# Optimization experiments

Hardware: AMD Instinct MI355X
Metric: run time of the kernel (lower is better)

Reference implementation:

```python
import jax, jax.numpy as jnp
import numpy as np
from jax import lax

B, S, T, H, VIN, VOUT = 32, 128, 64, 512, 32000, 32000
PAD_IDX = 1


def setup_inputs() -> dict:
    key = jax.random.key(0)
    ks = jax.random.split(key, 20)
    sc = 0.05
    rn = lambda k, shp: (jax.random.normal(k, shp, jnp.float32) * sc)
    return {
        "src": jax.random.randint(ks[0], (B, S), 0, VIN),
        "src_len": jnp.full((B,), S, dtype=jnp.int32),
        "trg": jax.random.randint(ks[1], (B, T), 0, VOUT),
        "enc_emb": rn(ks[2], (VIN, H)),
        "enc_wih": rn(ks[3], (4 * H, H)),
        "enc_whh": rn(ks[4], (4 * H, H)),
        "enc_bih": rn(ks[5], (4 * H,)),
        "enc_bhh": rn(ks[6], (4 * H,)),
        "enc_fc_w": rn(ks[7], (H, H)),
        "enc_fc_b": rn(ks[8], (H,)),
        "dec_emb": rn(ks[9], (VOUT, H)),
        "attn_w": rn(ks[10], (H, 2 * H)),
        "attn_b": rn(ks[11], (H,)),
        "attn_v": rn(ks[12], (H,)),
        "dec_wih": rn(ks[13], (4 * H, 2 * H)),
        "dec_whh": rn(ks[14], (4 * H, H)),
        "dec_bih": rn(ks[15], (4 * H,)),
        "dec_bhh": rn(ks[16], (4 * H,)),
        "out_w": rn(ks[17], (VOUT, 3 * H)),
        "out_b": rn(ks[18], (VOUT,)),
    }


def _lstm_cell(x, h, c, wih, whh, bih, bhh):
    # PyTorch gate order: i, f, g, o
    g = x @ wih.T + bih + h @ whh.T + bhh
    i, f, gg, o = jnp.split(g, 4, axis=-1)
    c = jax.nn.sigmoid(f) * c + jax.nn.sigmoid(i) * jnp.tanh(gg)
    h = jax.nn.sigmoid(o) * jnp.tanh(c)
    return h, c


def reference(src, src_len, trg, enc_emb, enc_wih, enc_whh, enc_bih, enc_bhh,
              enc_fc_w, enc_fc_b, dec_emb, attn_w, attn_b, attn_v,
              dec_wih, dec_whh, dec_bih, dec_bhh, out_w, out_b):
    b = src.shape[0]
    # ---- Encoder: single-layer LSTM over time (full lengths) ----
    emb = enc_emb[src].transpose(1, 0, 2)  # [S,B,H] time-major
    h0 = jnp.zeros((b, H), emb.dtype)
    c0 = jnp.zeros((b, H), emb.dtype)

    def enc_step(carry, x_t):
        h, c = carry
        h, c = _lstm_cell(x_t, h, c, enc_wih, enc_whh, enc_bih, enc_bhh)
        return (h, c), h

    (hf, cf), enc_out = lax.scan(enc_step, (h0, c0), emb)  # enc_out [S,B,H]
    hidden = jnp.tanh(hf @ enc_fc_w.T + enc_fc_b)  # [B,H]
    enc_bt = enc_out.transpose(1, 0, 2)  # [B,S,H]
    mask = src != PAD_IDX  # [B,S]

    # ---- Decoder: teacher forcing (ratio=1.0), scan over target steps ----
    def dec_step(carry, tok):
        h, c = carry
        e = dec_emb[tok]  # [B,H]
        # Bahdanau attention
        hrep = jnp.broadcast_to(h[:, None, :], enc_bt.shape)  # [B,S,H]
        energy = jnp.tanh(jnp.concatenate([hrep, enc_bt], -1) @ attn_w.T + attn_b)
        score = energy @ attn_v  # [B,S]
        score = jnp.where(mask, score, jnp.float32(-1e10))
        a = jax.nn.softmax(score, axis=1)
        weighted = jnp.einsum('bs,bsh->bh', a, enc_bt)  # [B,H]
        x = jnp.concatenate([e, weighted], -1)  # [B,2H]
        h, c = _lstm_cell(x, h, c, dec_wih, dec_whh, dec_bih, dec_bhh)
        pred = jnp.concatenate([h, weighted, e], -1) @ out_w.T + out_b  # [B,V]
        return (h, c), pred

    tokens = trg.T  # [T,B]
    (_, _), logits = lax.scan(dec_step, (hidden, cf), tokens[:-1])  # [T-1,B,V]
    outputs = jnp.concatenate(
        [jnp.zeros((1, b, VOUT), logits.dtype), logits], axis=0)  # [T,B,V]
    return outputs
```

## Files before the change

### kernel.cpp

```cpp
#include <hip/hip_runtime.h>

typedef unsigned short u16;
typedef unsigned int u32;
typedef unsigned long long u64;
typedef __attribute__((ext_vector_type(8))) short bf16x8;
typedef __attribute__((ext_vector_type(8))) unsigned short u16x8;
typedef __attribute__((ext_vector_type(4))) unsigned short u16x4;
typedef __attribute__((ext_vector_type(4))) float f32x4;

#define DEVI static __device__ __forceinline__
#define MFMA __builtin_amdgcn_mfma_f32_16x16x32_bf16

constexpr int B = 32, S = 128, T = 64, H = 512, V = 32000;
constexpr int H4 = 4 * H;
constexpr int TD = T - 1;
constexpr int MOUT = TD * B;
constexpr int KOUT = 3 * H;
constexpr int PAD_IDX = 1;

DEVI u16 f2bf(float f) {
  union { float f; unsigned u; } v; v.f = f;
  unsigned r = (v.u + 0x7fffu + ((v.u >> 16) & 1u)) >> 16;
  return (u16)r;
}
DEVI float bf2f(u16 h) {
  union { unsigned u; float f; } v; v.u = ((unsigned)h) << 16;
  return v.f;
}
DEVI float sigm(float x) { return 1.f / (1.f + __expf(-x)); }
DEVI float tanh_(float x) {
  float ax = fabsf(x);
  float e = __expf(-2.f * ax);
  float t = (1.f - e) / (1.f + e);
  return x < 0.f ? -t : t;
}
DEVI float tanhf_(float x) {
  float e = __expf(2.f * x);
  return 1.f - 2.f * __builtin_amdgcn_rcpf(e + 1.f);
}
DEVI int swz(int row, int k8) { return row * 32 + ((k8 ^ (row & 3)) << 3); }

DEVI u64 pack4u(const u16* p) {
  return (u64)p[0] | ((u64)p[1] << 16) | ((u64)p[2] << 32) | ((u64)p[3] << 48);
}
DEVI u64 xstore(u16* p, u64 v) {
  return __hip_atomic_exchange((u64*)p, v, __ATOMIC_RELAXED,
                               __HIP_MEMORY_SCOPE_AGENT);
}
DEVI void sstore(unsigned* p, unsigned v) {
  __hip_atomic_exchange(p, v, __ATOMIC_RELAXED, __HIP_MEMORY_SCOPE_AGENT);
}
DEVI void poll_bo(unsigned* p, unsigned tgt) {
  int it = 0;
  long long t0 = (long long)__builtin_amdgcn_s_memrealtime();
  while (__hip_atomic_load(p, __ATOMIC_RELAXED, __HIP_MEMORY_SCOPE_AGENT) <
         tgt) {
    if (it < 4) {
      __builtin_amdgcn_s_sleep(1);
      it++;
    } else {
      __builtin_amdgcn_s_sleep(8);
    }
    if ((long long)__builtin_amdgcn_s_memrealtime() - t0 > 20000000ll) break;
  }
}

__global__ __launch_bounds__(256) void gemm_bt(
    const u16* __restrict__ A, int lda,
    const u16* __restrict__ Bt, int ldb,
    float* __restrict__ C, int ldc,
    const float* __restrict__ bias, int M, int K, int bf16out) {
  __shared__ u16 As[128 * 32], Bs[128 * 32];
  const int tid = threadIdx.x;
  const int m0 = blockIdx.y * 128, n0 = blockIdx.x * 128;
  const int lane = tid & 63, w = tid >> 6, wm = w >> 1, wn = w & 1;
  const int lr = lane & 15, lk = lane >> 4;
  f32x4 acc[4][4] = {};
  const int r = tid >> 1, cc = (tid & 1) * 16, k8b = (tid & 1) * 2;

  for (int k0 = 0; k0 < K; k0 += 32) {
    {
      long gr = m0 + r;
      u16x8 v0 = {}, v1 = {};
      if (gr < M) {
        const u16* s = A + gr * (long)lda + k0 + cc;
        v0 = *(const u16x8*)s;
        v1 = *(const u16x8*)(s + 8);
      }
      *(u16x8*)&As[swz(r, k8b)] = v0;
      *(u16x8*)&As[swz(r, k8b + 1)] = v1;
    }
    {
      const u16* s = Bt + (long)(n0 + r) * ldb + k0 + cc;
      u16x8 v0 = *(const u16x8*)s;
      u16x8 v1 = *(const u16x8*)(s + 8);
      *(u16x8*)&Bs[swz(r, k8b)] = v0;
      *(u16x8*)&Bs[swz(r, k8b + 1)] = v1;
    }
    __syncthreads();
    bf16x8 af[4], bfr[4];
#pragma unroll
    for (int mi = 0; mi < 4; mi++)
      af[mi] = *(const bf16x8*)&As[swz(wm * 64 + mi * 16 + lr, lk)];
#pragma unroll
    for (int ni = 0; ni < 4; ni++)
      bfr[ni] = *(const bf16x8*)&Bs[swz(wn * 64 + ni * 16 + lr, lk)];
#pragma unroll
    for (int mi = 0; mi < 4; mi++)
#pragma unroll
      for (int ni = 0; ni < 4; ni++)
        acc[mi][ni] = MFMA(af[mi], bfr[ni], acc[mi][ni], 0, 0, 0);
    __syncthreads();
  }
#pragma unroll
  for (int ni = 0; ni < 4; ni++) {
    int col = n0 + wn * 64 + ni * 16 + lr;
    float bs = bias ? bias[col] : 0.f;
#pragma unroll
    for (int mi = 0; mi < 4; mi++) {
#pragma unroll
      for (int rr = 0; rr < 4; rr++) {
        long row = m0 + wm * 64 + mi * 16 + lk * 4 + rr;
        if (row < M) {
          float v = acc[mi][ni][rr] + bs;
          if (bf16out)
            ((u16*)C)[row * (long)ldc + col] = f2bf(v);
          else
            C[row * (long)ldc + col] = v;
        }
      }
    }
  }
}

__global__ void zero_f(float* p, long n) {
  long i = (long)blockIdx.x * 256 + threadIdx.x;
  long st = (long)gridDim.x * 256;
  for (; i < n; i += st) p[i] = 0.f;
}

__global__ void zero_u(unsigned* p, int n) {
  int i = blockIdx.x * 256 + threadIdx.x;
  if (i < n) p[i] = 0u;
}

__global__ void cast_bf(const float* __restrict__ src, u16* __restrict__ dst,
                        int ld, int off, int Csz) {
  long row = blockIdx.y;
  int col = blockIdx.x * 256 + threadIdx.x;
  dst[row * Csz + col] = f2bf(src[row * ld + off + col]);
}

__global__ void cast_bf4(const float* __restrict__ src, u16* __restrict__ dst,
                         long n4) {
  long i = (long)blockIdx.x * 256 + threadIdx.x;
  if (i >= n4) return;
  float4 v = ((const float4*)src)[i];
  u16x4 o;
  o[0] = f2bf(v.x); o[1] = f2bf(v.y); o[2] = f2bf(v.z); o[3] = f2bf(v.w);
  *(u16x4*)&dst[i * 4] = o;
}

__global__ void cast_perm(const float* __restrict__ src, int ld, int off,
                          u16* __restrict__ dst) {
  int np = blockIdx.y;
  int c = blockIdx.x * 256 + threadIdx.x;
  int g = np & 3, jH = np >> 2;
  dst[(size_t)np * H + c] = f2bf(src[(size_t)(g * H + jH) * ld + off + c]);
}

__global__ void pack_wdec_p(const float* __restrict__ wih,
                            const float* __restrict__ whh,
                            u16* __restrict__ dst) {
  int r = blockIdx.y;
  int k = blockIdx.x * 256 + threadIdx.x;
  int g = r & 3, j = r >> 2;
  int srow = g * H + j;
  float v = (k < 512) ? wih[(size_t)srow * (2 * H) + 512 + k]
                      : whh[(size_t)srow * H + (k - 512)];
  dst[(size_t)r * 1024 + k] = f2bf(v);
}

__global__ void bias_perm(const float* __restrict__ a,
                          const float* __restrict__ b, float* __restrict__ o) {
  int np = blockIdx.x * 256 + threadIdx.x;
  int g = np & 3, jH = np >> 2;
  int r = g * H + jH;
  o[np] = a[r] + b[r];
}

__global__ __launch_bounds__(256) void cast_transpose_bf(
    const float* __restrict__ src, int ld, int off, u16* __restrict__ dst,
    int R) {
  __shared__ float tile[32][33];
  int r0 = blockIdx.y * 32, c0 = blockIdx.x * 32;
  int tx = threadIdx.x & 31, ty = threadIdx.x >> 5;
#pragma unroll
  for (int i = 0; i < 32; i += 8)
    tile[ty + i][tx] = src[(long)(r0 + ty + i) * ld + off + c0 + tx];
  __syncthreads();
#pragma unroll
  for (int i = 0; i < 32; i += 8)
    dst[(long)(c0 + ty + i) * R + r0 + tx] = f2bf(tile[tx][ty + i]);
}

__global__ void gather_src_emb(const int* __restrict__ src,
                               const float* __restrict__ emb,
                               u16* __restrict__ dst) {
  int row = blockIdx.y;
  int t = row >> 5, b = row & 31;
  int c = blockIdx.x * 256 + threadIdx.x;
  int tok = src[b * S + t];
  dst[(long)row * H + c] = f2bf(emb[(long)tok * H + c]);
}

__global__ void gather_trg_emb(const int* __restrict__ trg,
                               const float* __restrict__ emb,
                               u16* __restrict__ xout) {
  int row = blockIdx.y;
  int t = row >> 5, b = row & 31;
  int c = blockIdx.x * 256 + threadIdx.x;
  int tok = trg[b * T + t];
  xout[(long)row * KOUT + 2 * H + c] = f2bf(emb[(long)tok * H + c]);
}

__global__ __launch_bounds__(512) void enc_persist32(
    unsigned* fes, const u16* __restrict__ wenc_p,
    const float* __restrict__ xih_p, u16* hstep, u16* enc_bt_bf, float* cbuf) {
  __shared__ float gs[32][64];
  __shared__ float c_s[512];
  __shared__ u16 hx[512];
  const int tid = threadIdx.x, bk = blockIdx.x;
  const int wave = tid >> 6, lane = tid & 63;
  const int lr = lane & 15, lk = lane >> 4;
  const int bq = tid >> 4, jl = tid & 15;
  c_s[tid] = 0.f;
  const int mt = wave & 1, nt = wave >> 1;
  const int n = nt * 16 + lr;
  bf16x8 wf[16];
  {
    const u16* wp = wenc_p + (size_t)(bk * 64 + n) * 512 + lk * 8;
#pragma unroll
    for (int kt = 0; kt < 16; kt++) wf[kt] = *(const bf16x8*)(wp + kt * 32);
  }
  for (int t = 0; t < S; t++) {
    if (t > 0 && tid < 32) poll_bo(fes + tid * 16, (unsigned)t);
    __syncthreads();
    float4 xv = *(const float4*)(xih_p + ((size_t)t * B + bq) * H4 +
                                 (bk * 16 + jl) * 4);
    {
      const u16* ab =
          hstep + (size_t)t * B * H + (size_t)(mt * 16 + lr) * H + lk * 8;
      f32x4 acc = {};
#pragma unroll
      for (int kt = 0; kt < 16; kt++) {
        bf16x8 a = *(const bf16x8*)(ab + kt * 32);
        acc = MFMA(a, wf[kt], acc, 0, 0, 0);
      }
#pragma unroll
      for (int rr = 0; rr < 4; rr++) gs[mt * 16 + lk * 4 + rr][n] = acc[rr];
    }
    __syncthreads();
    {
      float gi = xv.x + gs[bq][jl * 4 + 0];
      float gf = xv.y + gs[bq][jl * 4 + 1];
      float gg = xv.z + gs[bq][jl * 4 + 2];
      float go = xv.w + gs[bq][jl * 4 + 3];
      float cn = sigm(gf) * c_s[tid] + sigm(gi) * tanh_(gg);
      c_s[tid] = cn;
      u16 h16 = f2bf(sigm(go) * tanh_(cn));
      hx[tid] = h16;
      enc_bt_bf[((size_t)bq * S + t) * H + bk * 16 + jl] = h16;
    }
    __syncthreads();
    u64 kp = 0;
    if (tid < 128) {
      int bb = tid >> 2, q = tid & 3;
      kp = xstore(hstep + (size_t)(t + 1) * B * H + (size_t)bb * H + bk * 16 +
                      q * 4,
                  pack4u(&hx[bb * 16 + q * 4]));
    }
    if (wave < 2) {
      asm volatile("" :: "v"(kp));
      asm volatile("s_waitcnt vmcnt(0)" ::: "memory");
    }
    __syncthreads();
    if (tid == 0) sstore(fes + bk * 16, (unsigned)(t + 1));
  }
  cbuf[bq * H + bk * 16 + jl] = c_s[tid];
}

__global__ __launch_bounds__(512) void dec_persist32(
    unsigned* fhs, unsigned* fws, const float* __restrict__ fc_w,
    const float* __restrict__ fc_b, const u16* __restrict__ wdec_p,
    const u16* __restrict__ a1T_bf, const float* __restrict__ attn_v,
    const int* __restrict__ src, const u16* __restrict__ hf_bf,
    const float* __restrict__ cbuf, const u16* __restrict__ epart_bf,
    const u16* __restrict__ enc_bt_bf, const float* __restrict__ eih_p,
    u16* hstep, u16* wstep, u16* __restrict__ xout_bf) {
  __shared__ float buf[8][512];
  __shared__ float hs[512], hps[512];
  __shared__ float gh[32][64];
  __shared__ float gw[32][64];
  __shared__ float sc[128], red[2];
  __shared__ int smask[128];
  __shared__ float c_s[512];
  __shared__ u16 hx[512];
  const int tid = threadIdx.x, bk = blockIdx.x;
  const int wave = tid >> 6, lane = tid & 63;
  const int lr = lane & 15, lk = lane >> 4;
  const int bq = tid >> 4, jl = tid & 15;
  c_s[tid] = cbuf[bq * H + bk * 16 + jl];
  if (tid < 128) smask[tid] = src[bk * S + tid];
  float av8[8];
#pragma unroll
  for (int e = 0; e < 8; e++) av8[e] = attn_v[lane * 8 + e];
  if (wave < 2) {
    const u16* ab = hf_bf + (size_t)(wave * 16 + lr) * H + lk * 8;
    const float* frow = fc_w + (size_t)(bk * 16 + lr) * H + lk * 8;
    f32x4 acc = {};
#pragma unroll
    for (int kt = 0; kt < 16; kt++) {
      bf16x8 a = *(const bf16x8*)(ab + kt * 32);
      bf16x8 w;
#pragma unroll
      for (int e = 0; e < 8; e++) w[e] = (short)f2bf(frow[kt * 32 + e]);
      acc = MFMA(a, w, acc, 0, 0, 0);
    }
    float bs = fc_b[bk * 16 + lr];
#pragma unroll
    for (int rr = 0; rr < 4; rr++)
      hx[(wave * 16 + lk * 4 + rr) * 16 + lr] = f2bf(tanh_(acc[rr] + bs));
  }
  __syncthreads();
  {
    u64 kp = 0;
    if (tid < 128) {
      int bb = tid >> 2, q = tid & 3;
      kp = xstore(hstep + (size_t)bb * H + bk * 16 + q * 4,
                  pack4u(&hx[bb * 16 + q * 4]));
    }
    if (wave < 2) {
      asm volatile("" :: "v"(kp));
      asm volatile("s_waitcnt vmcnt(0)" ::: "memory");
    }
    __syncthreads();
    if (tid == 0) sstore(fhs + bk * 16, 1u);
  }
  const int mt = wave & 1, nt = wave >> 1;
  const int n = nt * 16 + lr;
  const u16* wpw = wdec_p + (size_t)(bk * 64 + n) * 1024 + lk * 8;
  const u16* wph = wpw + 512;
  bf16x8 wwf[16];
#pragma unroll
  for (int kt = 0; kt < 16; kt++) wwf[kt] = *(const bf16x8*)(wpw + kt * 32);
  for (int t = 0; t < TD; t++) {
    if (tid < 32) poll_bo(fhs + tid * 16, (unsigned)(t + 1));
    __syncthreads();
    float4 xv = *(const float4*)(eih_p + ((size_t)t * B + bq) * H4 +
                                 (bk * 16 + jl) * 4);
    {
      const u16* ah =
          hstep + (size_t)t * B * H + (size_t)(mt * 16 + lr) * H + lk * 8;
      f32x4 acc = {};
#pragma unroll
      for (int kt = 0; kt < 16; kt++) {
        bf16x8 a = *(const bf16x8*)(ah + kt * 32);
        bf16x8 w = *(const bf16x8*)(wph + kt * 32);
        acc = MFMA(a, w, acc, 0, 0, 0);
      }
#pragma unroll
      for (int rr = 0; rr < 4; rr++) gh[mt * 16 + lk * 4 + rr][n] = acc[rr];
    }
    if (tid < 256) {
      u32 v = ((const u32*)(hstep + (size_t)t * B * H + (size_t)bk * H))[tid];
      hs[2 * tid] = bf2f((u16)(v & 0xffff));
      hs[2 * tid + 1] = bf2f((u16)(v >> 16));
    }
    __syncthreads();
    {
      float p[8] = {};
      const int j0 = lane * 8;
#pragma unroll 8
      for (int kk = 0; kk < 64; kk++) {
        int k = wave * 64 + kk;
        float hk = hs[k];
        u16x8 av = *(const u16x8*)&a1T_bf[(size_t)k * H + j0];
#pragma unroll
        for (int e = 0; e < 8; e++) p[e] += hk * bf2f(av[e]);
      }
#pragma unroll
      for (int e = 0; e < 8; e++) buf[wave][j0 + e] = p[e];
    }
    __syncthreads();
    {
      float s0 = 0.f;
#pragma unroll
      for (int w = 0; w < 8; w++) s0 += buf[w][tid];
      hps[tid] = s0;
    }
    __syncthreads();
    {
      const int j0 = lane * 8;
      float hp8[8];
#pragma unroll
      for (int e = 0; e < 8; e++) hp8[e] = hps[j0 + e];
#pragma unroll 4
      for (int i = 0; i < 16; i++) {
        int s = wave * 16 + i;
        u16x8 ep = *(const u16x8*)&epart_bf[((size_t)bk * S + s) * H + j0];
        float a = 0.f;
#pragma unroll
        for (int e = 0; e < 8; e++) a += av8[e] * tanhf_(hp8[e] + bf2f(ep[e]));
#pragma unroll
        for (int o = 32; o; o >>= 1) a += __shfl_xor(a, o);
        if (lane == 0) sc[s] = (smask[s] == PAD_IDX) ? -1e10f : a;
      }
    }
    __syncthreads();
    if (tid < 64) {
      float v = fmaxf(sc[tid], sc[tid + 64]);
#pragma unroll
      for (int o = 32; o; o >>= 1) v = fmaxf(v, __shfl_xor(v, o));
      if (tid == 0) red[0] = v;
    }
    __syncthreads();
    float mx = red[0];
    if (tid < S) sc[tid] = __expf(sc[tid] - mx);
    __syncthreads();
    if (tid < 64) {
      float v = sc[tid] + sc[tid + 64];
#pragma unroll
      for (int o = 32; o; o >>= 1) v += __shfl_xor(v, o);
      if (tid == 0) red[1] = 1.f / v;
    }
    __syncthreads();
    {
      float acc8[8] = {};
      const int j0 = lane * 8;
#pragma unroll 4
      for (int i = 0; i < 16; i++) {
        int s = wave * 16 + i;
        float ps = sc[s];
        u16x8 ev = *(const u16x8*)&enc_bt_bf[((size_t)bk * S + s) * H + j0];
#pragma unroll
        for (int e = 0; e < 8; e++) acc8[e] += ps * bf2f(ev[e]);
      }
#pragma unroll
      for (int e = 0; e < 8; e++) buf[wave][j0 + e] = acc8[e];
    }
    __syncthreads();
    {
      u64 kp = 0;
      if (tid < 128) {
        float inv = red[1];
        int j0 = tid * 4;
        u16x4 o;
#pragma unroll
        for (int i = 0; i < 4; i++) {
          float wj = (buf[0][j0 + i] + buf[1][j0 + i] + buf[2][j0 + i] +
                      buf[3][j0 + i] + buf[4][j0 + i] + buf[5][j0 + i] +
                      buf[6][j0 + i] + buf[7][j0 + i]) *
                     inv;
          o[i] = f2bf(wj);
        }
        *(u16x4*)&xout_bf[((size_t)t * B + bk) * KOUT + H + j0] = o;
        u64 val = (u64)o[0] | ((u64)o[1] << 16) | ((u64)o[2] << 32) |
                  ((u64)o[3] << 48);
        kp = xstore(wstep + ((size_t)t * B + bk) * H + j0, val);
      }
      if (wave < 2) {
        asm volatile("" :: "v"(kp));
        asm volatile("s_waitcnt vmcnt(0)" ::: "memory");
      }
      __syncthreads();
      if (tid == 0) sstore(fws + bk * 16, (unsigned)(t + 1));
    }
    if (tid < 32) poll_bo(fws + tid * 16, (unsigned)(t + 1));
    __syncthreads();
    {
      const u16* aw =
          wstep + (size_t)t * B * H + (size_t)(mt * 16 + lr) * H + lk * 8;
      f32x4 acc = {};
#pragma unroll
      for (int kt = 0; kt < 16; kt++) {
        bf16x8 a = *(const bf16x8*)(aw + kt * 32);
        acc = MFMA(a, wwf[kt], acc, 0, 0, 0);
      }
#pragma unroll
      for (int rr = 0; rr < 4; rr++) gw[mt * 16 + lk * 4 + rr][n] = acc[rr];
    }
    __syncthreads();
    {
      float gi = xv.x + gh[bq][jl * 4 + 0] + gw[bq][jl * 4 + 0];
      float gf = xv.y + gh[bq][jl * 4 + 1] + gw[bq][jl * 4 + 1];
      float gg = xv.z + gh[bq][jl * 4 + 2] + gw[bq][jl * 4 + 2];
      float go = xv.w + gh[bq][jl * 4 + 3] + gw[bq][jl * 4 + 3];
      float cn = sigm(gf) * c_s[tid] + sigm(gi) * tanh_(gg);
      c_s[tid] = cn;
      u16 h16 = f2bf(sigm(go) * tanh_(cn));
      hx[tid] = h16;
      xout_bf[((size_t)t * B + bq) * KOUT + bk * 16 + jl] = h16;
    }
    __syncthreads();
    {
      u64 kp = 0;
      if (tid < 128) {
        int bb = tid >> 2, q = tid & 3;
        kp = xstore(hstep + (size_t)(t + 1) * B * H + (size_t)bb * H +
                        bk * 16 + q * 4,
                    pack4u(&hx[bb * 16 + q * 4]));
      }
      if (wave < 2) {
        asm volatile("" :: "v"(kp));
        asm volatile("s_waitcnt vmcnt(0)" ::: "memory");
      }
      __syncthreads();
      if (tid == 0) sstore(fhs + bk * 16, (unsigned)(t + 2));
    }
  }
}

extern "C" void kernel_launch(void* const* d_in, const int* in_sizes, int n_in,
                              void* d_out, int out_size, void* d_ws,
                              size_t ws_size, hipStream_t stream) {
  const int* src = (const int*)d_in[0];
  const int* trg = (const int*)d_in[2];
  const float* enc_emb = (const float*)d_in[3];
  const float* enc_wih = (const float*)d_in[4];
  const float* enc_whh = (const float*)d_in[5];
  const float* enc_bih = (const float*)d_in[6];
  const float* enc_bhh = (const float*)d_in[7];
  const float* fc_w = (const float*)d_in[8];
  const float* fc_b = (const float*)d_in[9];
  const float* dec_emb = (const float*)d_in[10];
  const float* attn_w = (const float*)d_in[11];
  const float* attn_b = (const float*)d_in[12];
  const float* attn_v = (const float*)d_in[13];
  const float* dec_wih = (const float*)d_in[14];
  const float* dec_whh = (const float*)d_in[15];
  const float* dec_bih = (const float*)d_in[16];
  const float* dec_bhh = (const float*)d_in[17];
  const float* out_w = (const float*)d_in[18];
  const float* out_b = (const float*)d_in[19];
  float* out = (float*)d_out;

  char* wp = (char*)d_ws;
  auto alloc = [&](size_t n) {
    char* p = wp;
    wp += (n + 255) & ~(size_t)255;
    return p;
  };
  u16* outw_bf = (u16*)alloc((size_t)V * KOUT * 2);
  u16* wihenc_p = (u16*)alloc((size_t)H4 * H * 2);
  u16* wihE_p = (u16*)alloc((size_t)H4 * H * 2);
  u16* wenc_p = (u16*)alloc((size_t)H4 * H * 2);
  u16* wdec_p = (u16*)alloc((size_t)H4 * 2 * H * 2);
  u16* attnw2_bf = (u16*)alloc((size_t)H * H * 2);
  u16* a1T_bf = (u16*)alloc((size_t)H * H * 2);
  u16* xemb_bf = (u16*)alloc((size_t)S * B * H * 2);
  float* xih_p = (float*)alloc((size_t)S * B * H4 * 4);
  u16* enc_bt_bf = (u16*)alloc((size_t)B * S * H * 2);
  u16* epart_bf = (u16*)alloc((size_t)B * S * H * 2);
  float* eih_p = (float*)alloc((size_t)MOUT * H4 * 4);
  u16* xout_bf = (u16*)alloc((size_t)MOUT * KOUT * 2);
  u16* hstep_enc = (u16*)alloc((size_t)(S + 1) * B * H * 2);
  u16* hstep_dec = (u16*)alloc((size_t)T * B * H * 2);
  u16* wstep = (u16*)alloc((size_t)TD * B * H * 2);
  float* cbuf = (float*)alloc((size_t)B * H * 4);
  float* benc_p = (float*)alloc((size_t)H4 * 4);
  float* bdec_p = (float*)alloc((size_t)H4 * 4);
  unsigned* flags = (unsigned*)alloc(2048 * 4);
  unsigned* fes = flags;
  unsigned* fhs = flags + 512;
  unsigned* fws = flags + 1024;

  dim3 blk(256);
  zero_f<<<dim3(256), blk, 0, stream>>>(out, (long)B * V);
  zero_u<<<dim3(8), blk, 0, stream>>>(flags, 2048);
  zero_u<<<dim3(32), blk, 0, stream>>>((unsigned*)hstep_enc, B * H / 2);
  cast_bf4<<<dim3(((long)V * KOUT / 4 + 255) / 256), blk, 0, stream>>>(
      out_w, outw_bf, (long)V * KOUT / 4);
  cast_perm<<<dim3(H / 256, H4), blk, 0, stream>>>(enc_wih, H, 0, wihenc_p);
  cast_perm<<<dim3(H / 256, H4), blk, 0, stream>>>(dec_wih, 2 * H, 0, wihE_p);
  cast_perm<<<dim3(H / 256, H4), blk, 0, stream>>>(enc_whh, H, 0, wenc_p);
  pack_wdec_p<<<dim3(4, H4), blk, 0, stream>>>(dec_wih, dec_whh, wdec_p);
  cast_bf<<<dim3(H / 256, H), blk, 0, stream>>>(attn_w, attnw2_bf, 2 * H, H, H);
  cast_transpose_bf<<<dim3(H / 32, H / 32), blk, 0, stream>>>(attn_w, 2 * H, 0,
                                                              a1T_bf, H);
  bias_perm<<<dim3(H4 / 256), blk, 0, stream>>>(enc_bih, enc_bhh, benc_p);
  bias_perm<<<dim3(H4 / 256), blk, 0, stream>>>(dec_bih, dec_bhh, bdec_p);
  gather_src_emb<<<dim3(H / 256, S * B), blk, 0, stream>>>(src, enc_emb,
                                                           xemb_bf);
  gather_trg_emb<<<dim3(H / 256, MOUT), blk, 0, stream>>>(trg, dec_emb,
                                                          xout_bf);
  gemm_bt<<<dim3(H4 / 128, (S * B) / 128), blk, 0, stream>>>(
      xemb_bf, H, wihenc_p, H, xih_p, H4, benc_p, S * B, H, 0);
  gemm_bt<<<dim3(H4 / 128, (MOUT + 127) / 128), blk, 0, stream>>>(
      xout_bf + 2 * H, KOUT, wihE_p, H, eih_p, H4, bdec_p, MOUT, H, 0);
  enc_persist32<<<dim3(32), dim3(512), 0, stream>>>(fes, wenc_p, xih_p,
                                                    hstep_enc, enc_bt_bf, cbuf);
  gemm_bt<<<dim3(H / 128, (B * S) / 128), blk, 0, stream>>>(
      enc_bt_bf, H, attnw2_bf, H, (float*)epart_bf, H, attn_b, B * S, H, 1);
  dec_persist32<<<dim3(32), dim3(512), 0, stream>>>(
      fhs, fws, fc_w, fc_b, wdec_p, a1T_bf, attn_v, src,
      hstep_enc + (size_t)S * B * H, cbuf, epart_bf, enc_bt_bf, eih_p,
      hstep_dec, wstep, xout_bf);
  gemm_bt<<<dim3(V / 128, (MOUT + 127) / 128), blk, 0, stream>>>(
      xout_bf, KOUT, outw_bf, KOUT, out + (size_t)B * V, V, out_b, MOUT, KOUT,
      0);
}
```

Baseline: 3.182 ms.

## Overlap side work with encoder recurrence and distribute decoder attention projection via MFMA

Result: faster. 2.934 ms (-7.8%).

```diff
diff --git a/kernel.cpp b/kernel.cpp
--- a/kernel.cpp
+++ b/kernel.cpp
@@ -45,6 +45,10 @@
 }
 DEVI u64 xstore(u16* p, u64 v) {
   return __hip_atomic_exchange((u64*)p, v, __ATOMIC_RELAXED,
+                               __HIP_MEMORY_SCOPE_AGENT);
+}
+DEVI u64 xstore64(u64* p, u64 v) {
+  return __hip_atomic_exchange(p, v, __ATOMIC_RELAXED,
                                __HIP_MEMORY_SCOPE_AGENT);
 }
 DEVI void sstore(unsigned* p, unsigned v) {
@@ -59,7 +63,7 @@
       __builtin_amdgcn_s_sleep(1);
       it++;
     } else {
-      __builtin_amdgcn_s_sleep(8);
+      __builtin_amdgcn_s_sleep(4);
     }
     if ((long long)__builtin_amdgcn_s_memrealtime() - t0 > 20000000ll) break;
   }
@@ -133,6 +137,73 @@
   }
 }
 
+DEVI void gemm_tile512(const u16* A, int lda, const u16* Bt, int ldb,
+                       float* C, int ldc, const float* bias, int M, int K,
+                       int mt, int nt) {
+  __shared__ u16 As[128 * 32], Bs[128 * 32];
+  const int tid = threadIdx.x;
+  const bool act = tid < 256;
+  const int m0 = mt * 128, n0 = nt * 128;
+  const int lane = tid & 63, w = tid >> 6, wm = (w >> 1) & 1, wn = w & 1;
+  const int lr = lane & 15, lk = lane >> 4;
+  f32x4 acc[4][4] = {};
+  const int r = (tid >> 1) & 127, cc = (tid & 1) * 16, k8b = (tid & 1) * 2;
+
+  for (int k0 = 0; k0 < K; k0 += 32) {
+    if (act) {
+      {
+        long gr = m0 + r;
+        u16x8 v0 = {}, v1 = {};
+        if (gr < M) {
+          const u16* s = A + gr * (long)lda + k0 + cc;
+          v0 = *(const u16x8*)s;
+          v1 = *(const u16x8*)(s + 8);
+        }
+        *(u16x8*)&As[swz(r, k8b)] = v0;
+        *(u16x8*)&As[swz(r, k8b + 1)] = v1;
+      }
+      {
+        const u16* s = Bt + (long)(n0 + r) * ldb + k0 + cc;
+        u16x8 v0 = *(const u16x8*)s;
+        u16x8 v1 = *(const u16x8*)(s + 8);
+        *(u16x8*)&Bs[swz(r, k8b)] = v0;
+        *(u16x8*)&Bs[swz(r, k8b + 1)] = v1;
+      }
+    }
+    __syncthreads();
+    if (act) {
+      bf16x8 af[4], bfr[4];
+#pragma unroll
+      for (int mi = 0; mi < 4; mi++)
+        af[mi] = *(const bf16x8*)&As[swz(wm * 64 + mi * 16 + lr, lk)];
+#pragma unroll
+      for (int ni = 0; ni < 4; ni++)
+        bfr[ni] = *(const bf16x8*)&Bs[swz(wn * 64 + ni * 16 + lr, lk)];
+#pragma unroll
+      for (int mi = 0; mi < 4; mi++)
+#pragma unroll
+        for (int ni = 0; ni < 4; ni++)
+          acc[mi][ni] = MFMA(af[mi], bfr[ni], acc[mi][ni], 0, 0, 0);
+    }
+    __syncthreads();
+  }
+  if (act) {
+#pragma unroll
+    for (int ni = 0; ni < 4; ni++) {
+      int col = n0 + wn * 64 + ni * 16 + lr;
+      float bs = bias ? bias[col] : 0.f;
+#pragma unroll
+      for (int mi = 0; mi < 4; mi++) {
+#pragma unroll
+        for (int rr = 0; rr < 4; rr++) {
+          long row = m0 + wm * 64 + mi * 16 + lk * 4 + rr;
+          if (row < M) C[row * (long)ldc + col] = acc[mi][ni][rr] + bs;
+        }
+      }
+    }
+  }
+}
+
 __global__ void zero_f(float* p, long n) {
   long i = (long)blockIdx.x * 256 + threadIdx.x;
   long st = (long)gridDim.x * 256;
@@ -149,16 +220,6 @@
   long row = blockIdx.y;
   int col = blockIdx.x * 256 + threadIdx.x;
   dst[row * Csz + col] = f2bf(src[row * ld + off + col]);
-}
-
-__global__ void cast_bf4(const float* __restrict__ src, u16* __restrict__ dst,
-                         long n4) {
-  long i = (long)blockIdx.x * 256 + threadIdx.x;
-  if (i >= n4) return;
-  float4 v = ((const float4*)src)[i];
-  u16x4 o;
-  o[0] = f2bf(v.x); o[1] = f2bf(v.y); o[2] = f2bf(v.z); o[3] = f2bf(v.w);
-  *(u16x4*)&dst[i * 4] = o;
 }
 
 __global__ void cast_perm(const float* __restrict__ src, int ld, int off,
@@ -189,21 +250,6 @@
   o[np] = a[r] + b[r];
 }
 
-__global__ __launch_bounds__(256) void cast_transpose_bf(
-    const float* __restrict__ src, int ld, int off, u16* __restrict__ dst,
-    int R) {
-  __shared__ float tile[32][33];
-  int r0 = blockIdx.y * 32, c0 = blockIdx.x * 32;
-  int tx = threadIdx.x & 31, ty = threadIdx.x >> 5;
-#pragma unroll
-  for (int i = 0; i < 32; i += 8)
-    tile[ty + i][tx] = src[(long)(r0 + ty + i) * ld + off + c0 + tx];
-  __syncthreads();
-#pragma unroll
-  for (int i = 0; i < 32; i += 8)
-    dst[(long)(c0 + ty + i) * R + r0 + tx] = f2bf(tile[tx][ty + i]);
-}
-
 __global__ void gather_src_emb(const int* __restrict__ src,
                                const float* __restrict__ emb,
                                u16* __restrict__ dst) {
@@ -224,13 +270,33 @@
   xout[(long)row * KOUT + 2 * H + c] = f2bf(emb[(long)tok * H + c]);
 }
 
-__global__ __launch_bounds__(512) void enc_persist32(
+__global__ __launch_bounds__(512) void enc_fused(
     unsigned* fes, const u16* __restrict__ wenc_p,
-    const float* __restrict__ xih_p, u16* hstep, u16* enc_bt_bf, float* cbuf) {
+    const float* __restrict__ xih_p, u16* hstep, u16* enc_bt_bf, float* cbuf,
+    const u16* __restrict__ xoute, const u16* __restrict__ wihE_p,
+    float* __restrict__ eih_p, const float* __restrict__ bdec_p,
+    const float* __restrict__ out_w, u16* __restrict__ outw_bf) {
+  const int bk = blockIdx.x;
+  if (bk >= 288) {
+    long i = (long)(bk - 288) * 512 + threadIdx.x;
+    const long n4 = (long)V * KOUT / 4, st = 96L * 512;
+    for (; i < n4; i += st) {
+      float4 v = ((const float4*)out_w)[i];
+      u16x4 o;
+      o[0] = f2bf(v.x); o[1] = f2bf(v.y); o[2] = f2bf(v.z); o[3] = f2bf(v.w);
+      *(u16x4*)&outw_bf[i * 4] = o;
+    }
+    return;
+  }
+  if (bk >= 32) {
+    int job = bk - 32, mt = job >> 4, nt = job & 15;
+    gemm_tile512(xoute, KOUT, wihE_p, H, eih_p, H4, bdec_p, MOUT, H, mt, nt);
+    return;
+  }
   __shared__ float gs[32][64];
   __shared__ float c_s[512];
   __shared__ u16 hx[512];
-  const int tid = threadIdx.x, bk = blockIdx.x;
+  const int tid = threadIdx.x;
   const int wave = tid >> 6, lane = tid & 63;
   const int lr = lane & 15, lk = lane >> 4;
   const int bq = tid >> 4, jl = tid & 15;
@@ -291,15 +357,16 @@
 }
 
 __global__ __launch_bounds__(512) void dec_persist32(
-    unsigned* fhs, unsigned* fws, const float* __restrict__ fc_w,
+    unsigned* fhs, unsigned* fws, unsigned* fps, const float* __restrict__ fc_w,
     const float* __restrict__ fc_b, const u16* __restrict__ wdec_p,
-    const u16* __restrict__ a1T_bf, const float* __restrict__ attn_v,
+    const u16* __restrict__ a1_bf, const float* __restrict__ attn_v,
     const int* __restrict__ src, const u16* __restrict__ hf_bf,
     const float* __restrict__ cbuf, const u16* __restrict__ epart_bf,
     const u16* __restrict__ enc_bt_bf, const float* __restrict__ eih_p,
-    u16* hstep, u16* wstep, u16* __restrict__ xout_bf) {
+    u16* hstep, u16* wstep, float* hpstep, u16* __restrict__ xout_bf) {
   __shared__ float buf[8][512];
-  __shared__ float hs[512], hps[512];
+  __shared__ float hps[512];
+  __shared__ float hp2[32][16];
   __shared__ float gh[32][64];
   __shared__ float gw[32][64];
   __shared__ float sc[128], red[2];
@@ -372,33 +439,41 @@
 #pragma unroll
       for (int rr = 0; rr < 4; rr++) gh[mt * 16 + lk * 4 + rr][n] = acc[rr];
     }
-    if (tid < 256) {
-      u32 v = ((const u32*)(hstep + (size_t)t * B * H + (size_t)bk * H))[tid];
-      hs[2 * tid] = bf2f((u16)(v & 0xffff));
-      hs[2 * tid + 1] = bf2f((u16)(v >> 16));
-    }
-    __syncthreads();
-    {
-      float p[8] = {};
-      const int j0 = lane * 8;
-#pragma unroll 8
-      for (int kk = 0; kk < 64; kk++) {
-        int k = wave * 64 + kk;
-        float hk = hs[k];
-        u16x8 av = *(const u16x8*)&a1T_bf[(size_t)k * H + j0];
-#pragma unroll
-        for (int e = 0; e < 8; e++) p[e] += hk * bf2f(av[e]);
-      }
-#pragma unroll
-      for (int e = 0; e < 8; e++) buf[wave][j0 + e] = p[e];
-    }
-    __syncthreads();
-    {
-      float s0 = 0.f;
-#pragma unroll
-      for (int w = 0; w < 8; w++) s0 += buf[w][tid];
-      hps[tid] = s0;
-    }
+    if (wave < 2) {
+      const u16* ah =
+          hstep + (size_t)t * B * H + (size_t)(wave * 16 + lr) * H + lk * 8;
+      const u16* bp = a1_bf + (size_t)(bk * 16 + lr) * 512 + lk * 8;
+      f32x4 acc = {};
+#pragma unroll
+      for (int kt = 0; kt < 16; kt++) {
+        bf16x8 a = *(const bf16x8*)(ah + kt * 32);
+        bf16x8 w = *(const bf16x8*)(bp + kt * 32);
+        acc = MFMA(a, w, acc, 0, 0, 0);
+      }
+#pragma unroll
+      for (int rr = 0; rr < 4; rr++)
+        hp2[wave * 16 + lk * 4 + rr][lr] = acc[rr];
+    }
+    __syncthreads();
+    {
+      u64 kp = 0;
+      if (tid < 256) {
+        int b = tid >> 3, ql = tid & 7;
+        u64 pk = (u64)__float_as_uint(hp2[b][ql * 2]) |
+                 ((u64)__float_as_uint(hp2[b][ql * 2 + 1]) << 32);
+        kp = xstore64(
+            (u64*)(hpstep + ((size_t)t * B + b) * 512 + bk * 16 + ql * 2), pk);
+      }
+      if (wave < 4) {
+        asm volatile("" :: "v"(kp));
+        asm volatile("s_waitcnt vmcnt(0)" ::: "memory");
+      }
+      __syncthreads();
+      if (tid == 0) sstore(fps + bk * 16, (unsigned)(t + 1));
+    }
+    if (tid < 32) poll_bo(fps + tid * 16, (unsigned)(t + 1));
+    __syncthreads();
+    hps[tid] = hpstep[((size_t)t * B + bk) * 512 + tid];
     __syncthreads();
     {
       const int j0 = lane * 8;
@@ -425,11 +500,12 @@
       if (tid == 0) red[0] = v;
     }
     __syncthreads();
-    float mx = red[0];
-    if (tid < S) sc[tid] = __expf(sc[tid] - mx);
-    __syncthreads();
     if (tid < 64) {
-      float v = sc[tid] + sc[tid + 64];
+      float mx = red[0];
+      float e0 = __expf(sc[tid] - mx), e1 = __expf(sc[tid + 64] - mx);
+      sc[tid] = e0;
+      sc[tid + 64] = e1;
+      float v = e0 + e1;
 #pragma unroll
       for (int o = 32; o; o >>= 1) v += __shfl_xor(v, o);
       if (tid == 0) red[1] = 1.f / v;
@@ -557,7 +633,7 @@
   u16* wenc_p = (u16*)alloc((size_t)H4 * H * 2);
   u16* wdec_p = (u16*)alloc((size_t)H4 * 2 * H * 2);
   u16* attnw2_bf = (u16*)alloc((size_t)H * H * 2);
-  u16* a1T_bf = (u16*)alloc((size_t)H * H * 2);
+  u16* a1_bf = (u16*)alloc((size_t)H * H * 2);
   u16* xemb_bf = (u16*)alloc((size_t)S * B * H * 2);
   float* xih_p = (float*)alloc((size_t)S * B * H4 * 4);
   u16* enc_bt_bf = (u16*)alloc((size_t)B * S * H * 2);
@@ -567,6 +643,7 @@
   u16* hstep_enc = (u16*)alloc((size_t)(S + 1) * B * H * 2);
   u16* hstep_dec = (u16*)alloc((size_t)T * B * H * 2);
   u16* wstep = (u16*)alloc((size_t)TD * B * H * 2);
+  float* hpstep = (float*)alloc((size_t)TD * B * H * 4);
   float* cbuf = (float*)alloc((size_t)B * H * 4);
   float* benc_p = (float*)alloc((size_t)H4 * 4);
   float* bdec_p = (float*)alloc((size_t)H4 * 4);
@@ -574,20 +651,18 @@
   unsigned* fes = flags;
   unsigned* fhs = flags + 512;
   unsigned* fws = flags + 1024;
+  unsigned* fps = flags + 1536;
 
   dim3 blk(256);
   zero_f<<<dim3(256), blk, 0, stream>>>(out, (long)B * V);
   zero_u<<<dim3(8), blk, 0, stream>>>(flags, 2048);
   zero_u<<<dim3(32), blk, 0, stream>>>((unsigned*)hstep_enc, B * H / 2);
-  cast_bf4<<<dim3(((long)V * KOUT / 4 + 255) / 256), blk, 0, stream>>>(
-      out_w, outw_bf, (long)V * KOUT / 4);
   cast_perm<<<dim3(H / 256, H4), blk, 0, stream>>>(enc_wih, H, 0, wihenc_p);
   cast_perm<<<dim3(H / 256, H4), blk, 0, stream>>>(dec_wih, 2 * H, 0, wihE_p);
   cast_perm<<<dim3(H / 256, H4), blk, 0, stream>>>(enc_whh, H, 0, wenc_p);
   pack_wdec_p<<<dim3(4, H4), blk, 0, stream>>>(dec_wih, dec_whh, wdec_p);
   cast_bf<<<dim3(H / 256, H), blk, 0, stream>>>(attn_w, attnw2_bf, 2 * H, H, H);
-  cast_transpose_bf<<<dim3(H / 32, H / 32), blk, 0, stream>>>(attn_w, 2 * H, 0,
-                                                              a1T_bf, H);
+  cast_bf<<<dim3(H / 256, H), blk, 0, stream>>>(attn_w, a1_bf, 2 * H, 0, H);
   bias_perm<<<dim3(H4 / 256), blk, 0, stream>>>(enc_bih, enc_bhh, benc_p);
   bias_perm<<<dim3(H4 / 256), blk, 0, stream>>>(dec_bih, dec_bhh, bdec_p);
   gather_src_emb<<<dim3(H / 256, S * B), blk, 0, stream>>>(src, enc_emb,
@@ -596,16 +671,15 @@
                                                           xout_bf);
   gemm_bt<<<dim3(H4 / 128, (S * B) / 128), blk, 0, stream>>>(
       xemb_bf, H, wihenc_p, H, xih_p, H4, benc_p, S * B, H, 0);
-  gemm_bt<<<dim3(H4 / 128, (MOUT + 127) / 128), blk, 0, stream>>>(
-      xout_bf + 2 * H, KOUT, wihE_p, H, eih_p, H4, bdec_p, MOUT, H, 0);
-  enc_persist32<<<dim3(32), dim3(512), 0, stream>>>(fes, wenc_p, xih_p,
-                                                    hstep_enc, enc_bt_bf, cbuf);
+  enc_fused<<<dim3(384), dim3(512), 0, stream>>>(
+      fes, wenc_p, xih_p, hstep_enc, enc_bt_bf, cbuf, xout_bf + 2 * H, wihE_p,
+      eih_p, bdec_p, out_w, outw_bf);
   gemm_bt<<<dim3(H / 128, (B * S) / 128), blk, 0, stream>>>(
       enc_bt_bf, H, attnw2_bf, H, (float*)epart_bf, H, attn_b, B * S, H, 1);
   dec_persist32<<<dim3(32), dim3(512), 0, stream>>>(
-      fhs, fws, fc_w, fc_b, wdec_p, a1T_bf, attn_v, src,
+      fhs, fws, fps, fc_w, fc_b, wdec_p, a1_bf, attn_v, src,
       hstep_enc + (size_t)S * B * H, cbuf, epart_bf, enc_bt_bf, eih_p,
-      hstep_dec, wstep, xout_bf);
+      hstep_dec, wstep, hpstep, xout_bf);
   gemm_bt<<<dim3(V / 128, (MOUT + 127) / 128), blk, 0, stream>>>(
       xout_bf, KOUT, outw_bf, KOUT, out + (size_t)B * V, V, out_b, MOUT, KOUT,
       0);
```
